# Optimization experiments

Measured on AMD Instinct MI355X. Metric: run time of the kernel, lower is better.

The kernel has to match this reference:

```python
import jax, jax.numpy as jnp
import numpy as np

NC = 1_000_000   # children
NP_ = 100_000    # parents
DIM = 64         # value/channel dim
H = 4            # heads
DQK = 8          # per-head query/key dim
DH = DQK * H     # 32
RPE = 9          # edge_attr feature dim
SCALE = DQK ** -0.5


def setup_inputs() -> dict:
    key = jax.random.key(0)
    ks = jax.random.split(key, 12)
    return {
        "x_child": jax.random.normal(ks[0], (NC, DIM), dtype=jnp.float32),
        "x_parent": jax.random.normal(ks[1], (NP_, DIM), dtype=jnp.float32),
        "index": jax.random.randint(ks[2], (NC,), 0, NP_, dtype=jnp.int64),
        "edge_attr": jax.random.normal(ks[3], (NC, RPE), dtype=jnp.float32),
        "wq": jax.random.normal(ks[4], (DIM, DH), dtype=jnp.float32) * 0.05,
        "bq": jax.random.normal(ks[5], (DH,), dtype=jnp.float32) * 0.05,
        "wkv": jax.random.normal(ks[6], (DIM, DH + DIM), dtype=jnp.float32) * 0.05,
        "bkv": jax.random.normal(ks[7], (DH + DIM,), dtype=jnp.float32) * 0.05,
        "wk_rpe": jax.random.normal(ks[8], (RPE, DH), dtype=jnp.float32) * 0.05,
        "bk_rpe": jax.random.normal(ks[9], (DH,), dtype=jnp.float32) * 0.05,
        "wq_rpe": jax.random.normal(ks[10], (RPE, DH), dtype=jnp.float32) * 0.05,
        "bq_rpe": jax.random.normal(ks[11], (DH,), dtype=jnp.float32) * 0.05,
    }


def reference(x_child, x_parent, index, edge_attr,
              wq, bq, wkv, bkv, wk_rpe, bk_rpe, wq_rpe, bq_rpe):
    Nc = x_child.shape[0]
    Np = x_parent.shape[0]
    # _get_query: Linear(Cp -> H*DQK) on parents, then gather per child edge
    q_parent = x_parent @ wq + bq                      # (Np, H*D)
    q = q_parent[index].reshape(Nc, H, DQK) * SCALE    # (Nc, H, D)
    # kv projection on children
    kv = x_child @ wkv + bkv                           # (Nc, H*D + DIM)
    k = kv[:, :DH].reshape(Nc, H, DQK)
    v = kv[:, DH:].reshape(Nc, H, DIM // H)
    # relative positional encodings added to k and q
    k = k + (edge_attr @ wk_rpe + bk_rpe).reshape(Nc, H, DQK)
    q = q + (edge_attr @ wq_rpe + bq_rpe).reshape(Nc, H, DQK)
    # per-edge compatibility, segment softmax grouped by parent index
    compat = jnp.einsum('nhd,nhd->nh', q, k)           # (Nc, H)
    m = jax.ops.segment_max(compat, index, num_segments=Np)   # (Np, H)
    e = jnp.exp(compat - m[index])
    s = jax.ops.segment_sum(e, index, num_segments=Np)        # (Np, H)
    attn = e / (s[index] + 1e-16)                      # (Nc, H)
    # weighted scatter-sum pooling
    xw = (v * attn[:, :, None]).reshape(Nc, DIM)       # (Nc, DIM)
    out = jax.ops.segment_sum(xw, index, num_segments=Np)     # (Np, DIM)
    return out
```

## Files before the change

kernel.cpp:

```cpp
#include <hip/hip_runtime.h>

#define NC    1000000
#define NPAR  100000
#define DIM   64
#define H     4
#define RPE   9
#define SCALE 0.35355339059327373f
#define CB    128
#define NBS   ((NPAR + 1023) / 1024)

typedef __attribute__((ext_vector_type(8))) short short8;
typedef __attribute__((ext_vector_type(4))) float f32x4;

__device__ inline unsigned short f2bf(float f) {
    unsigned int u = __float_as_uint(f);
    u += 0x7fff + ((u >> 16) & 1);
    return (unsigned short)(u >> 16);
}
__device__ inline unsigned int pack2bf(float a, float b) {
    return (unsigned int)f2bf(a) | ((unsigned int)f2bf(b) << 16);
}

__global__ __launch_bounds__(256) void qproj_kernel(const float* __restrict__ xp,
                             const float* __restrict__ wq,
                             const float* __restrict__ bq,
                             float* __restrict__ qp) {
    __shared__ float wqT[32 * 64];
    __shared__ float bqL[32];
    int tid = threadIdx.x;
    for (int i = tid; i < 2048; i += 256) { int o = i >> 6, j = i & 63; wqT[i] = wq[j * 32 + o]; }
    if (tid < 32) bqL[tid] = bq[tid];
    __syncthreads();
    int p = blockIdx.x * 256 + tid;
    if (p >= NPAR) return;
    float4 x4[16];
    const float4* xr = (const float4*)(xp + (size_t)p * 64);
#pragma unroll
    for (int i = 0; i < 16; ++i) x4[i] = xr[i];
    float* qpr = qp + (size_t)p * 32;
#pragma unroll 1
    for (int o = 0; o < 32; ++o) {
        float acc = bqL[o];
        const float4* w4 = (const float4*)(wqT + o * 64);
#pragma unroll
        for (int j = 0; j < 16; ++j) { float4 w = w4[j], xx = x4[j];
            acc += xx.x * w.x + xx.y * w.y + xx.z * w.z + xx.w * w.w; }
        qpr[o] = acc * SCALE;
    }
}

__global__ __launch_bounds__(256) void prepB_kernel(
    const float* __restrict__ wkv, const float* __restrict__ bkv,
    const float* __restrict__ wkr, const float* __restrict__ bkr,
    const float* __restrict__ wqr, const float* __restrict__ bqr,
    uint4* __restrict__ Bg) {
    int tid = threadIdx.x;
    for (int i = tid; i < 12 * 128; i += 256) {
        int kb = i >> 7, n = i & 127;
        float w[8];
#pragma unroll
        for (int jj = 0; jj < 8; ++jj) {
            int k = kb * 8 + jj;
            float val = 0.f;
            if (n < 32) {
                if (k < 64)       val = wkv[k * 96 + n];
                else if (k < 73)  val = wkr[(k - 64) * 32 + n];
                else if (k == 73) val = bkv[n] + bkr[n];
            } else if (n < 96) {
                int d = n - 32;
                if (k < 64)       val = wkv[k * 96 + 32 + d];
                else if (k == 73) val = bkv[32 + d];
            } else {
                int o = n - 96;
                if (k >= 64 && k < 73) val = wqr[(k - 64) * 32 + o];
                else if (k == 73)      val = bqr[o];
            }
            w[jj] = val;
        }
        uint4 v;
        v.x = pack2bf(w[0], w[1]); v.y = pack2bf(w[2], w[3]);
        v.z = pack2bf(w[4], w[5]); v.w = pack2bf(w[6], w[7]);
        Bg[kb * 128 + n] = v;
    }
}

__global__ __launch_bounds__(256) void hist_kernel(const int* __restrict__ index,
                            int* __restrict__ cnt) {
    int c = blockIdx.x * 256 + threadIdx.x;
    if (c >= NC) return;
    atomicAdd(&cnt[index[c]], 1);
}

__global__ __launch_bounds__(1024) void scanA_kernel(const int* __restrict__ cnt,
                                                     int* __restrict__ bsum) {
    __shared__ int red[16];
    int i = blockIdx.x * 1024 + threadIdx.x;
    int v = (i < NPAR) ? cnt[i] : 0;
#pragma unroll
    for (int off = 32; off; off >>= 1) v += __shfl_down(v, off, 64);
    if ((threadIdx.x & 63) == 0) red[threadIdx.x >> 6] = v;
    __syncthreads();
    if (threadIdx.x < 16) {
        int s = red[threadIdx.x];
#pragma unroll
        for (int off = 8; off; off >>= 1) s += __shfl_down(s, off, 16);
        if (threadIdx.x == 0) bsum[blockIdx.x] = s;
    }
}

__global__ __launch_bounds__(128) void scanB_kernel(int* __restrict__ bsum) {
    __shared__ int s[128];
    int t = threadIdx.x;
    int v = (t < NBS) ? bsum[t] : 0;
    s[t] = v;
    __syncthreads();
    for (int off = 1; off < 128; off <<= 1) {
        int x = s[t];
        int add = (t >= off) ? s[t - off] : 0;
        __syncthreads();
        s[t] = x + add;
        __syncthreads();
    }
    if (t < NBS) bsum[t] = s[t] - v;
}

__global__ __launch_bounds__(1024) void scanC_kernel(const int* __restrict__ cnt,
                                                     const int* __restrict__ bsum,
                                                     int* __restrict__ rowStart,
                                                     int* __restrict__ cursor) {
    __shared__ int s[1024];
    int t = threadIdx.x;
    int i = blockIdx.x * 1024 + t;
    int v = (i < NPAR) ? cnt[i] : 0;
    s[t] = v;
    __syncthreads();
    for (int off = 1; off < 1024; off <<= 1) {
        int x = s[t];
        int add = (t >= off) ? s[t - off] : 0;
        __syncthreads();
        s[t] = x + add;
        __syncthreads();
    }
    int excl = s[t] - v + bsum[blockIdx.x];
    if (i < NPAR) { rowStart[i] = excl; cursor[i] = excl; }
    if (i == NPAR - 1) rowStart[NPAR] = excl + v;
}

__global__ __launch_bounds__(256) void scatter_kernel(const int* __restrict__ index,
                               int* __restrict__ cursor,
                               int2* __restrict__ ordCP) {
    int c = blockIdx.x * 256 + threadIdx.x;
    if (c >= NC) return;
    int p = index[c];
    int pos = atomicAdd(&cursor[p], 1);
    ordCP[pos] = make_int2(c, p);
}

__global__ __launch_bounds__(256, 4) void fused_kernel(
    const float* __restrict__ xc, const float* __restrict__ ea_g,
    const int2* __restrict__ ordCP,
    const int* __restrict__ rowStart,
    const uint4* __restrict__ Bg,
    const float* __restrict__ qp,
    float* __restrict__ outw, float* __restrict__ sW)
{
    __shared__ __align__(16) char R1[34816];
    __shared__ float e_lds[CB * 4];
    __shared__ int par_s[CB];
    __shared__ int wcnt[4];
    __shared__ int segStart[130];

    uint4* A4 = (uint4*)R1;
    float* wvS = (float*)R1;

    const int tid  = threadIdx.x;
    const int lane = tid & 63, wave = tid >> 6;
    const int col  = lane & 15, quad = lane >> 4;
    const int G    = blockIdx.x * CB;
    const int validCB = min(NC - G, CB);

    {
        const int half = tid >> 7;
        const int c = tid & 127;
        const bool valid = c < validCB;
        int ch = 0, p = 0x7fffffff;
        if (valid) { int2 cp = ordCP[G + c]; ch = cp.x; p = cp.y; }
        if (half == 0) {
            par_s[c] = p;
            float4 x4[10];
            if (valid) {
                const float4* xr = (const float4*)(xc + (size_t)ch * 64);
#pragma unroll
                for (int i = 0; i < 10; ++i) x4[i] = xr[i];
            } else {
#pragma unroll
                for (int i = 0; i < 10; ++i) x4[i] = make_float4(0.f, 0.f, 0.f, 0.f);
            }
#pragma unroll
            for (int kb = 0; kb < 5; ++kb) {
                uint4 v;
                v.x = pack2bf(x4[kb * 2].x, x4[kb * 2].y);
                v.y = pack2bf(x4[kb * 2].z, x4[kb * 2].w);
                v.z = pack2bf(x4[kb * 2 + 1].x, x4[kb * 2 + 1].y);
                v.w = pack2bf(x4[kb * 2 + 1].z, x4[kb * 2 + 1].w);
                A4[kb * 128 + c] = v;
            }
        } else {
            float4 x4[6];
            float ear[9];
            if (valid) {
                const float4* xr = (const float4*)(xc + (size_t)ch * 64);
#pragma unroll
                for (int i = 0; i < 6; ++i) x4[i] = xr[10 + i];
                const float* er = ea_g + (size_t)ch * 9;
#pragma unroll
                for (int r = 0; r < 9; ++r) ear[r] = er[r];
            } else {
#pragma unroll
                for (int i = 0; i < 6; ++i) x4[i] = make_float4(0.f, 0.f, 0.f, 0.f);
#pragma unroll
                for (int r = 0; r < 9; ++r) ear[r] = 0.f;
            }
#pragma unroll
            for (int kb = 0; kb < 3; ++kb) {
                uint4 v;
                v.x = pack2bf(x4[kb * 2].x, x4[kb * 2].y);
                v.y = pack2bf(x4[kb * 2].z, x4[kb * 2].w);
                v.z = pack2bf(x4[kb * 2 + 1].x, x4[kb * 2 + 1].y);
                v.w = pack2bf(x4[kb * 2 + 1].z, x4[kb * 2 + 1].w);
                A4[(5 + kb) * 128 + c] = v;
            }
            {
                uint4 v;
                v.x = pack2bf(ear[0], ear[1]); v.y = pack2bf(ear[2], ear[3]);
                v.z = pack2bf(ear[4], ear[5]); v.w = pack2bf(ear[6], ear[7]);
                A4[8 * 128 + c] = v;
            }
            {
                uint4 v;
                v.x = pack2bf(ear[8], valid ? 1.f : 0.f);
                v.y = 0u; v.z = 0u; v.w = 0u;
                A4[9 * 128 + c] = v;
            }
        }
    }
    __syncthreads();

    f32x4 acc[2][8];
#pragma unroll
    for (int mt = 0; mt < 2; ++mt)
#pragma unroll
        for (int nt = 0; nt < 8; ++nt) acc[mt][nt] = (f32x4){0.f, 0.f, 0.f, 0.f};
    const int wbase = wave * 32;
    const short8* As = (const short8*)A4;
    const short8* Bs = (const short8*)Bg;
    const short8 zero8 = {0, 0, 0, 0, 0, 0, 0, 0};
#pragma unroll 1
    for (int ks = 0; ks < 3; ++ks) {
        const int kb = ks * 4 + quad;
        short8 af0 = zero8, af1 = zero8;
        if (kb < 10) {
            af0 = As[kb * 128 + wbase + col];
            af1 = As[kb * 128 + wbase + 16 + col];
        }
        short8 bf[8];
#pragma unroll
        for (int nt = 0; nt < 6; ++nt) bf[nt] = Bs[kb * 128 + nt * 16 + col];
#pragma unroll
        for (int nt = 0; nt < 6; ++nt) {
            acc[0][nt] = __builtin_amdgcn_mfma_f32_16x16x32_bf16(af0, bf[nt], acc[0][nt], 0, 0, 0);
            acc[1][nt] = __builtin_amdgcn_mfma_f32_16x16x32_bf16(af1, bf[nt], acc[1][nt], 0, 0, 0);
        }
        if (ks == 2) {
#pragma unroll
            for (int nt = 6; nt < 8; ++nt) {
                short8 b2 = Bs[kb * 128 + nt * 16 + col];
                acc[0][nt] = __builtin_amdgcn_mfma_f32_16x16x32_bf16(af0, b2, acc[0][nt], 0, 0, 0);
                acc[1][nt] = __builtin_amdgcn_mfma_f32_16x16x32_bf16(af1, b2, acc[1][nt], 0, 0, 0);
            }
        }
    }
    __syncthreads();

    {
        float comp[2][4][2];
#pragma unroll
        for (int mt = 0; mt < 2; ++mt) {
#pragma unroll
            for (int r = 0; r < 4; ++r) {
                int cc = wbase + mt * 16 + quad * 4 + r;
                int p = par_s[cc];
                if (p >= NPAR) p = 0;
                const float* qpr = qp + (size_t)p * 32;
#pragma unroll
                for (int nt = 0; nt < 2; ++nt) {
                    float q = qpr[nt * 16 + col] + acc[mt][nt + 6][r];
                    comp[mt][r][nt] = acc[mt][nt][r] * q;
                }
            }
        }
#pragma unroll
        for (int m = 1; m < 8; m <<= 1) {
#pragma unroll
            for (int mt = 0; mt < 2; ++mt)
#pragma unroll
                for (int r = 0; r < 4; ++r)
#pragma unroll
                    for (int nt = 0; nt < 2; ++nt)
                        comp[mt][r][nt] += __shfl_xor(comp[mt][r][nt], m, 64);
        }
        {
            int idx = col & 7;
            int mtS = idx >> 2, rS = idx & 3;
            int cS = wbase + mtS * 16 + quad * 4 + rS;
            int hb = col >> 3;
            bool v0 = cS < validCB;
            e_lds[cS * 4 + hb]     = v0 ? __expf(comp[mtS][rS][0]) : 0.f;
            e_lds[cS * 4 + 2 + hb] = v0 ? __expf(comp[mtS][rS][1]) : 0.f;
        }
        const int c = tid;
        bool valid = (c < validCB);
        bool ishead = valid && (c == 0 || par_s[c - 1] != par_s[c]);
        unsigned long long mask = __ballot(ishead);
        if (lane == 0) wcnt[wave] = __popcll(mask);
        __syncthreads();
        int base = 0;
#pragma unroll
        for (int w = 0; w < 4; ++w) if (w < wave) base += wcnt[w];
        if (ishead) segStart[base + __popcll(mask & ((1ull << lane) - 1))] = c;
        if (tid == 0) {
            int ns = wcnt[0] + wcnt[1] + wcnt[2] + wcnt[3];
            segStart[ns] = validCB;
            segStart[129] = ns;
        }
    }

#pragma unroll
    for (int mt = 0; mt < 2; ++mt) {
        int cb = wbase + mt * 16 + quad * 4;
#pragma unroll
        for (int nt = 2; nt < 6; ++nt) {
            int d = (nt - 2) * 16 + col;
            int h = nt - 2;
#pragma unroll
            for (int r = 0; r < 4; ++r) {
                float e = e_lds[(cb + r) * 4 + h];
                wvS[(cb + r) * 68 + d] = acc[mt][nt][r] * e;
            }
        }
    }
    __syncthreads();

    {
        int nseg = segStart[129];
        for (int s = wave; s < nseg; s += 4) {
            int a = segStart[s], b = segStart[s + 1];
            int p = par_s[a];
            int d = lane, h = lane >> 4;
            float vs = 0.f, es = 0.f;
            for (int c2 = a; c2 < b; ++c2) {
                vs += wvS[c2 * 68 + d];
                es += e_lds[c2 * 4 + h];
            }
            bool full = (rowStart[p] == G + a) && (rowStart[p + 1] == G + b);
            if (full) {
                outw[(size_t)p * 64 + d] = vs;
                if ((d & 15) == 0) sW[(size_t)p * 4 + h] = es;
            } else {
                atomicAdd(&outw[(size_t)p * 64 + d], vs);
                if ((d & 15) == 0) atomicAdd(&sW[(size_t)p * 4 + h], es);
            }
        }
    }
}

__global__ __launch_bounds__(256) void norm_kernel(const float* __restrict__ sW,
                                                   float* __restrict__ out) {
    int t = blockIdx.x * 256 + threadIdx.x;
    if (t >= NPAR * 64) return;
    out[t] = out[t] / (sW[(t >> 6) * 4 + ((t >> 4) & 3)] + 1e-16f);
}

extern "C" void kernel_launch(void* const* d_in, const int* in_sizes, int n_in,
                              void* d_out, int out_size, void* d_ws, size_t ws_size,
                              hipStream_t stream) {
    const float* xc   = (const float*)d_in[0];
    const float* xp   = (const float*)d_in[1];
    const int*   idx  = (const int*)d_in[2];
    const float* ea   = (const float*)d_in[3];
    const float* wq   = (const float*)d_in[4];
    const float* bq   = (const float*)d_in[5];
    const float* wkv  = (const float*)d_in[6];
    const float* bkv  = (const float*)d_in[7];
    const float* wkr  = (const float*)d_in[8];
    const float* bkr  = (const float*)d_in[9];
    const float* wqr  = (const float*)d_in[10];
    const float* bqr  = (const float*)d_in[11];
    float* out = (float*)d_out;

    char* base = (char*)d_ws;
    size_t off = 0;
    auto alloc = [&](size_t bytes) {
        void* r = base + off;
        off += (bytes + 255) & ~(size_t)255;
        return r;
    };
    float* qp       = (float*)alloc((size_t)NPAR * 32 * sizeof(float));
    int*   cnt      = (int*)  alloc((size_t)NPAR * sizeof(int));
    int*   rowStart = (int*)  alloc(((size_t)NPAR + 1) * sizeof(int));
    int*   cursor   = (int*)  alloc((size_t)NPAR * sizeof(int));
    int2*  ordCP    = (int2*) alloc((size_t)NC * sizeof(int2));
    float* sW       = (float*)alloc((size_t)NPAR * 4 * sizeof(float));
    int*   bsum     = (int*)  alloc((size_t)NBS * sizeof(int));
    uint4* Bg       = (uint4*)alloc((size_t)12 * 128 * sizeof(uint4));
    (void)ws_size;

    hipMemsetAsync(cnt, 0, (size_t)NPAR * sizeof(int), stream);
    hipMemsetAsync(sW,  0, (size_t)NPAR * 4 * sizeof(float), stream);
    hipMemsetAsync(out, 0, (size_t)NPAR * 64 * sizeof(float), stream);

    qproj_kernel  <<<(NPAR + 255) / 256, 256, 0, stream>>>(xp, wq, bq, qp);
    prepB_kernel  <<<1,                  256, 0, stream>>>(wkv, bkv, wkr, bkr, wqr, bqr, Bg);
    hist_kernel   <<<(NC + 255) / 256,   256, 0, stream>>>(idx, cnt);
    scanA_kernel  <<<NBS,               1024, 0, stream>>>(cnt, bsum);
    scanB_kernel  <<<1,                  128, 0, stream>>>(bsum);
    scanC_kernel  <<<NBS,               1024, 0, stream>>>(cnt, bsum, rowStart, cursor);
    scatter_kernel<<<(NC + 255) / 256,   256, 0, stream>>>(idx, cursor, ordCP);
    fused_kernel  <<<(NC + CB - 1) / CB, 256, 0, stream>>>(xc, ea, ordCP, rowStart,
                                                           Bg, qp, out, sW);
    norm_kernel   <<<(NPAR * 64 + 255) / 256, 256, 0, stream>>>(sW, out);
}
```

Before: 677.9 us.

## Make fused kernel persistent with register prefetch of next tile's gathered rows

The fused attention kernel now runs as a persistent grid of 1024 blocks that loop over 128-child tiles. While the MFMA and epilogue work for the current tile runs, the next tile's ordCP entry, child features and edge attributes are loaded and packed to bf16 in registers. This is meant to hide the latency of the random-row gather behind compute. In exchange it raises register pressure, which may lower occupancy, and adds a barrier at the end of each tile.

```diff
diff --git a/kernel.cpp b/kernel.cpp
--- a/kernel.cpp
+++ b/kernel.cpp
@@ -8,6 +8,8 @@
 #define SCALE 0.35355339059327373f
 #define CB    128
 #define NBS   ((NPAR + 1023) / 1024)
+#define NT_TILES ((NC + CB - 1) / CB)
+#define GRID_F 1024
 
 typedef __attribute__((ext_vector_type(8))) short short8;
 typedef __attribute__((ext_vector_type(4))) float f32x4;
@@ -176,201 +178,257 @@
     const int tid  = threadIdx.x;
     const int lane = tid & 63, wave = tid >> 6;
     const int col  = lane & 15, quad = lane >> 4;
-    const int G    = blockIdx.x * CB;
-    const int validCB = min(NC - G, CB);
+    const int c    = tid & 127;
+    const int half = tid >> 7;
+    const int wbase = wave * 32;
+    const short8 zero8 = {0, 0, 0, 0, 0, 0, 0, 0};
+
+    int t = blockIdx.x;
+    int2 cp;
+    uint4 pk[5];
 
     {
-        const int half = tid >> 7;
-        const int c = tid & 127;
-        const bool valid = c < validCB;
-        int ch = 0, p = 0x7fffffff;
-        if (valid) { int2 cp = ordCP[G + c]; ch = cp.x; p = cp.y; }
+        int g = t * CB + c;
+        bool v = g < NC;
+        int2 cl = ordCP[v ? g : 0];
+        if (!v) { cl.x = 0; cl.y = 0x7fffffff; }
+        int ch = cl.x;
+        float4 xa[10]; float ear[9];
         if (half == 0) {
-            par_s[c] = p;
-            float4 x4[10];
-            if (valid) {
-                const float4* xr = (const float4*)(xc + (size_t)ch * 64);
-#pragma unroll
-                for (int i = 0; i < 10; ++i) x4[i] = xr[i];
-            } else {
-#pragma unroll
-                for (int i = 0; i < 10; ++i) x4[i] = make_float4(0.f, 0.f, 0.f, 0.f);
-            }
+            const float4* xr = (const float4*)(xc + (size_t)ch * 64);
+#pragma unroll
+            for (int i = 0; i < 10; ++i) xa[i] = xr[i];
 #pragma unroll
             for (int kb = 0; kb < 5; ++kb) {
-                uint4 v;
-                v.x = pack2bf(x4[kb * 2].x, x4[kb * 2].y);
-                v.y = pack2bf(x4[kb * 2].z, x4[kb * 2].w);
-                v.z = pack2bf(x4[kb * 2 + 1].x, x4[kb * 2 + 1].y);
-                v.w = pack2bf(x4[kb * 2 + 1].z, x4[kb * 2 + 1].w);
-                A4[kb * 128 + c] = v;
+                uint4 u;
+                u.x = pack2bf(xa[kb*2].x,   xa[kb*2].y);
+                u.y = pack2bf(xa[kb*2].z,   xa[kb*2].w);
+                u.z = pack2bf(xa[kb*2+1].x, xa[kb*2+1].y);
+                u.w = pack2bf(xa[kb*2+1].z, xa[kb*2+1].w);
+                pk[kb] = v ? u : make_uint4(0u,0u,0u,0u);
             }
         } else {
-            float4 x4[6];
-            float ear[9];
-            if (valid) {
-                const float4* xr = (const float4*)(xc + (size_t)ch * 64);
-#pragma unroll
-                for (int i = 0; i < 6; ++i) x4[i] = xr[10 + i];
-                const float* er = ea_g + (size_t)ch * 9;
-#pragma unroll
-                for (int r = 0; r < 9; ++r) ear[r] = er[r];
-            } else {
-#pragma unroll
-                for (int i = 0; i < 6; ++i) x4[i] = make_float4(0.f, 0.f, 0.f, 0.f);
-#pragma unroll
-                for (int r = 0; r < 9; ++r) ear[r] = 0.f;
-            }
+            const float4* xr = (const float4*)(xc + (size_t)ch * 64);
+#pragma unroll
+            for (int i = 0; i < 6; ++i) xa[i] = xr[10 + i];
+            const float* er = ea_g + (size_t)ch * 9;
+#pragma unroll
+            for (int r = 0; r < 9; ++r) ear[r] = er[r];
 #pragma unroll
             for (int kb = 0; kb < 3; ++kb) {
-                uint4 v;
-                v.x = pack2bf(x4[kb * 2].x, x4[kb * 2].y);
-                v.y = pack2bf(x4[kb * 2].z, x4[kb * 2].w);
-                v.z = pack2bf(x4[kb * 2 + 1].x, x4[kb * 2 + 1].y);
-                v.w = pack2bf(x4[kb * 2 + 1].z, x4[kb * 2 + 1].w);
-                A4[(5 + kb) * 128 + c] = v;
-            }
-            {
-                uint4 v;
-                v.x = pack2bf(ear[0], ear[1]); v.y = pack2bf(ear[2], ear[3]);
-                v.z = pack2bf(ear[4], ear[5]); v.w = pack2bf(ear[6], ear[7]);
-                A4[8 * 128 + c] = v;
-            }
-            {
-                uint4 v;
-                v.x = pack2bf(ear[8], valid ? 1.f : 0.f);
-                v.y = 0u; v.z = 0u; v.w = 0u;
-                A4[9 * 128 + c] = v;
-            }
-        }
-    }
-    __syncthreads();
-
-    f32x4 acc[2][8];
-#pragma unroll
-    for (int mt = 0; mt < 2; ++mt)
-#pragma unroll
-        for (int nt = 0; nt < 8; ++nt) acc[mt][nt] = (f32x4){0.f, 0.f, 0.f, 0.f};
-    const int wbase = wave * 32;
-    const short8* As = (const short8*)A4;
-    const short8* Bs = (const short8*)Bg;
-    const short8 zero8 = {0, 0, 0, 0, 0, 0, 0, 0};
-#pragma unroll 1
-    for (int ks = 0; ks < 3; ++ks) {
-        const int kb = ks * 4 + quad;
-        short8 af0 = zero8, af1 = zero8;
-        if (kb < 10) {
-            af0 = As[kb * 128 + wbase + col];
-            af1 = As[kb * 128 + wbase + 16 + col];
-        }
-        short8 bf[8];
-#pragma unroll
-        for (int nt = 0; nt < 6; ++nt) bf[nt] = Bs[kb * 128 + nt * 16 + col];
-#pragma unroll
-        for (int nt = 0; nt < 6; ++nt) {
-            acc[0][nt] = __builtin_amdgcn_mfma_f32_16x16x32_bf16(af0, bf[nt], acc[0][nt], 0, 0, 0);
-            acc[1][nt] = __builtin_amdgcn_mfma_f32_16x16x32_bf16(af1, bf[nt], acc[1][nt], 0, 0, 0);
-        }
-        if (ks == 2) {
-#pragma unroll
-            for (int nt = 6; nt < 8; ++nt) {
-                short8 b2 = Bs[kb * 128 + nt * 16 + col];
-                acc[0][nt] = __builtin_amdgcn_mfma_f32_16x16x32_bf16(af0, b2, acc[0][nt], 0, 0, 0);
-                acc[1][nt] = __builtin_amdgcn_mfma_f32_16x16x32_bf16(af1, b2, acc[1][nt], 0, 0, 0);
-            }
-        }
-    }
-    __syncthreads();
-
-    {
-        float comp[2][4][2];
+                uint4 u;
+                u.x = pack2bf(xa[kb*2].x,   xa[kb*2].y);
+                u.y = pack2bf(xa[kb*2].z,   xa[kb*2].w);
+                u.z = pack2bf(xa[kb*2+1].x, xa[kb*2+1].y);
+                u.w = pack2bf(xa[kb*2+1].z, xa[kb*2+1].w);
+                pk[kb] = v ? u : make_uint4(0u,0u,0u,0u);
+            }
+            uint4 u8;
+            u8.x = pack2bf(ear[0], ear[1]); u8.y = pack2bf(ear[2], ear[3]);
+            u8.z = pack2bf(ear[4], ear[5]); u8.w = pack2bf(ear[6], ear[7]);
+            pk[3] = v ? u8 : make_uint4(0u,0u,0u,0u);
+            uint4 u9;
+            u9.x = pack2bf(ear[8], 1.f); u9.y = 0u; u9.z = 0u; u9.w = 0u;
+            pk[4] = v ? u9 : make_uint4(0u,0u,0u,0u);
+        }
+        cp = cl;
+    }
+
+    for (; t < NT_TILES; t += GRID_F) {
+        const int G = t * CB;
+        const int validCB = min(NC - G, CB);
+
+        int tn = (t + GRID_F < NT_TILES) ? (t + GRID_F) : t;
+        int gn = tn * CB + c;
+        bool vn = gn < NC;
+        int2 cpn = ordCP[vn ? gn : 0];
+
+        if (half == 0) {
+            par_s[c] = cp.y;
+#pragma unroll
+            for (int kb = 0; kb < 5; ++kb) A4[kb * 128 + c] = pk[kb];
+        } else {
+#pragma unroll
+            for (int kb = 0; kb < 5; ++kb) A4[(5 + kb) * 128 + c] = pk[kb];
+        }
+        __syncthreads();
+
+        f32x4 acc[2][8];
+#pragma unroll
+        for (int mt = 0; mt < 2; ++mt)
+#pragma unroll
+            for (int nt = 0; nt < 8; ++nt) acc[mt][nt] = (f32x4){0.f, 0.f, 0.f, 0.f};
+        const short8* As = (const short8*)A4;
+        const short8* Bs = (const short8*)Bg;
+#pragma unroll
+        for (int ks = 0; ks < 3; ++ks) {
+            const int kb = ks * 4 + quad;
+            short8 af0 = zero8, af1 = zero8;
+            if (kb < 10) {
+                af0 = As[kb * 128 + wbase + col];
+                af1 = As[kb * 128 + wbase + 16 + col];
+            }
+            short8 bf[4];
+#pragma unroll
+            for (int nt = 0; nt < 4; ++nt) bf[nt] = Bs[kb * 128 + nt * 16 + col];
+#pragma unroll
+            for (int nt = 0; nt < 4; ++nt) {
+                acc[0][nt] = __builtin_amdgcn_mfma_f32_16x16x32_bf16(af0, bf[nt], acc[0][nt], 0, 0, 0);
+                acc[1][nt] = __builtin_amdgcn_mfma_f32_16x16x32_bf16(af1, bf[nt], acc[1][nt], 0, 0, 0);
+            }
+            bf[0] = Bs[kb * 128 + 4 * 16 + col];
+            bf[1] = Bs[kb * 128 + 5 * 16 + col];
+            acc[0][4] = __builtin_amdgcn_mfma_f32_16x16x32_bf16(af0, bf[0], acc[0][4], 0, 0, 0);
+            acc[1][4] = __builtin_amdgcn_mfma_f32_16x16x32_bf16(af1, bf[0], acc[1][4], 0, 0, 0);
+            acc[0][5] = __builtin_amdgcn_mfma_f32_16x16x32_bf16(af0, bf[1], acc[0][5], 0, 0, 0);
+            acc[1][5] = __builtin_amdgcn_mfma_f32_16x16x32_bf16(af1, bf[1], acc[1][5], 0, 0, 0);
+            if (ks == 2) {
+                bf[2] = Bs[kb * 128 + 6 * 16 + col];
+                bf[3] = Bs[kb * 128 + 7 * 16 + col];
+                acc[0][6] = __builtin_amdgcn_mfma_f32_16x16x32_bf16(af0, bf[2], acc[0][6], 0, 0, 0);
+                acc[1][6] = __builtin_amdgcn_mfma_f32_16x16x32_bf16(af1, bf[2], acc[1][6], 0, 0, 0);
+                acc[0][7] = __builtin_amdgcn_mfma_f32_16x16x32_bf16(af0, bf[3], acc[0][7], 0, 0, 0);
+                acc[1][7] = __builtin_amdgcn_mfma_f32_16x16x32_bf16(af1, bf[3], acc[1][7], 0, 0, 0);
+            }
+        }
+
+        int chn = vn ? cpn.x : 0;
+        float4 xa[10]; float ear[9];
+        if (half == 0) {
+            const float4* xr = (const float4*)(xc + (size_t)chn * 64);
+#pragma unroll
+            for (int i = 0; i < 10; ++i) xa[i] = xr[i];
+        } else {
+            const float4* xr = (const float4*)(xc + (size_t)chn * 64);
+#pragma unroll
+            for (int i = 0; i < 6; ++i) xa[i] = xr[10 + i];
+            const float* er = ea_g + (size_t)chn * 9;
+#pragma unroll
+            for (int r = 0; r < 9; ++r) ear[r] = er[r];
+        }
+
 #pragma unroll
         for (int mt = 0; mt < 2; ++mt) {
+            float comp[4][2];
 #pragma unroll
             for (int r = 0; r < 4; ++r) {
                 int cc = wbase + mt * 16 + quad * 4 + r;
                 int p = par_s[cc];
-                if (p >= NPAR) p = 0;
+                p = (p < NPAR) ? p : 0;
                 const float* qpr = qp + (size_t)p * 32;
 #pragma unroll
-                for (int nt = 0; nt < 2; ++nt) {
-                    float q = qpr[nt * 16 + col] + acc[mt][nt + 6][r];
-                    comp[mt][r][nt] = acc[mt][nt][r] * q;
+                for (int nt = 0; nt < 2; ++nt)
+                    comp[r][nt] = acc[mt][nt][r] * (qpr[nt * 16 + col] + acc[mt][nt + 6][r]);
+            }
+#pragma unroll
+            for (int m = 1; m < 8; m <<= 1)
+#pragma unroll
+                for (int r = 0; r < 4; ++r)
+#pragma unroll
+                    for (int nt = 0; nt < 2; ++nt)
+                        comp[r][nt] += __shfl_xor(comp[r][nt], m, 64);
+            int collo = lane & 7, colhi = (lane >> 3) & 1;
+            float eArg = comp[0][0];
+            eArg = (collo == 1) ? comp[1][0] : eArg;
+            eArg = (collo == 2) ? comp[2][0] : eArg;
+            eArg = (collo == 3) ? comp[3][0] : eArg;
+            eArg = (collo == 4) ? comp[0][1] : eArg;
+            eArg = (collo == 5) ? comp[1][1] : eArg;
+            eArg = (collo == 6) ? comp[2][1] : eArg;
+            eArg = (collo == 7) ? comp[3][1] : eArg;
+            int rS = collo & 3, ntS = collo >> 2;
+            int cS = wbase + mt * 16 + quad * 4 + rS;
+            float eV = (cS < validCB) ? __expf(eArg) : 0.f;
+            e_lds[cS * 4 + ntS * 2 + colhi] = eV;
+        }
+
+        if (half == 0) {
+#pragma unroll
+            for (int kb = 0; kb < 5; ++kb) {
+                uint4 u;
+                u.x = pack2bf(xa[kb*2].x,   xa[kb*2].y);
+                u.y = pack2bf(xa[kb*2].z,   xa[kb*2].w);
+                u.z = pack2bf(xa[kb*2+1].x, xa[kb*2+1].y);
+                u.w = pack2bf(xa[kb*2+1].z, xa[kb*2+1].w);
+                pk[kb] = vn ? u : make_uint4(0u,0u,0u,0u);
+            }
+        } else {
+#pragma unroll
+            for (int kb = 0; kb < 3; ++kb) {
+                uint4 u;
+                u.x = pack2bf(xa[kb*2].x,   xa[kb*2].y);
+                u.y = pack2bf(xa[kb*2].z,   xa[kb*2].w);
+                u.z = pack2bf(xa[kb*2+1].x, xa[kb*2+1].y);
+                u.w = pack2bf(xa[kb*2+1].z, xa[kb*2+1].w);
+                pk[kb] = vn ? u : make_uint4(0u,0u,0u,0u);
+            }
+            uint4 u8;
+            u8.x = pack2bf(ear[0], ear[1]); u8.y = pack2bf(ear[2], ear[3]);
+            u8.z = pack2bf(ear[4], ear[5]); u8.w = pack2bf(ear[6], ear[7]);
+            pk[3] = vn ? u8 : make_uint4(0u,0u,0u,0u);
+            uint4 u9;
+            u9.x = pack2bf(ear[8], 1.f); u9.y = 0u; u9.z = 0u; u9.w = 0u;
+            pk[4] = vn ? u9 : make_uint4(0u,0u,0u,0u);
+        }
+        cp.x = chn; cp.y = vn ? cpn.y : 0x7fffffff;
+
+        {
+            bool valid = (c == tid) && (tid < validCB);
+            bool vld = (tid < validCB);
+            bool ishead = vld && (tid == 0 || par_s[tid - 1] != par_s[tid]);
+            (void)valid;
+            unsigned long long mask = __ballot(ishead);
+            if (lane == 0) wcnt[wave] = __popcll(mask);
+            __syncthreads();
+            int base = 0;
+#pragma unroll
+            for (int w = 0; w < 4; ++w) if (w < wave) base += wcnt[w];
+            if (ishead) segStart[base + __popcll(mask & ((1ull << lane) - 1))] = tid;
+            if (tid == 0) {
+                int ns = wcnt[0] + wcnt[1] + wcnt[2] + wcnt[3];
+                segStart[ns] = validCB;
+                segStart[129] = ns;
+            }
+        }
+
+#pragma unroll
+        for (int mt = 0; mt < 2; ++mt) {
+            int cb = wbase + mt * 16 + quad * 4;
+#pragma unroll
+            for (int nt = 2; nt < 6; ++nt) {
+                int d = (nt - 2) * 16 + col;
+                int h = nt - 2;
+#pragma unroll
+                for (int r = 0; r < 4; ++r) {
+                    float e = e_lds[(cb + r) * 4 + h];
+                    wvS[(cb + r) * 68 + d] = acc[mt][nt][r] * e;
                 }
             }
         }
-#pragma unroll
-        for (int m = 1; m < 8; m <<= 1) {
-#pragma unroll
-            for (int mt = 0; mt < 2; ++mt)
-#pragma unroll
-                for (int r = 0; r < 4; ++r)
-#pragma unroll
-                    for (int nt = 0; nt < 2; ++nt)
-                        comp[mt][r][nt] += __shfl_xor(comp[mt][r][nt], m, 64);
-        }
+        __syncthreads();
+
         {
-            int idx = col & 7;
-            int mtS = idx >> 2, rS = idx & 3;
-            int cS = wbase + mtS * 16 + quad * 4 + rS;
-            int hb = col >> 3;
-            bool v0 = cS < validCB;
-            e_lds[cS * 4 + hb]     = v0 ? __expf(comp[mtS][rS][0]) : 0.f;
-            e_lds[cS * 4 + 2 + hb] = v0 ? __expf(comp[mtS][rS][1]) : 0.f;
-        }
-        const int c = tid;
-        bool valid = (c < validCB);
-        bool ishead = valid && (c == 0 || par_s[c - 1] != par_s[c]);
-        unsigned long long mask = __ballot(ishead);
-        if (lane == 0) wcnt[wave] = __popcll(mask);
-        __syncthreads();
-        int base = 0;
-#pragma unroll
-        for (int w = 0; w < 4; ++w) if (w < wave) base += wcnt[w];
-        if (ishead) segStart[base + __popcll(mask & ((1ull << lane) - 1))] = c;
-        if (tid == 0) {
-            int ns = wcnt[0] + wcnt[1] + wcnt[2] + wcnt[3];
-            segStart[ns] = validCB;
-            segStart[129] = ns;
-        }
-    }
-
-#pragma unroll
-    for (int mt = 0; mt < 2; ++mt) {
-        int cb = wbase + mt * 16 + quad * 4;
-#pragma unroll
-        for (int nt = 2; nt < 6; ++nt) {
-            int d = (nt - 2) * 16 + col;
-            int h = nt - 2;
-#pragma unroll
-            for (int r = 0; r < 4; ++r) {
-                float e = e_lds[(cb + r) * 4 + h];
-                wvS[(cb + r) * 68 + d] = acc[mt][nt][r] * e;
-            }
-        }
-    }
-    __syncthreads();
-
-    {
-        int nseg = segStart[129];
-        for (int s = wave; s < nseg; s += 4) {
-            int a = segStart[s], b = segStart[s + 1];
-            int p = par_s[a];
-            int d = lane, h = lane >> 4;
-            float vs = 0.f, es = 0.f;
-            for (int c2 = a; c2 < b; ++c2) {
-                vs += wvS[c2 * 68 + d];
-                es += e_lds[c2 * 4 + h];
-            }
-            bool full = (rowStart[p] == G + a) && (rowStart[p + 1] == G + b);
-            if (full) {
-                outw[(size_t)p * 64 + d] = vs;
-                if ((d & 15) == 0) sW[(size_t)p * 4 + h] = es;
-            } else {
-                atomicAdd(&outw[(size_t)p * 64 + d], vs);
-                if ((d & 15) == 0) atomicAdd(&sW[(size_t)p * 4 + h], es);
-            }
-        }
+            int nseg = segStart[129];
+            for (int s = wave; s < nseg; s += 4) {
+                int a = segStart[s], b = segStart[s + 1];
+                int p = par_s[a];
+                int d = lane, h = lane >> 4;
+                float vs = 0.f, es = 0.f;
+                for (int c2 = a; c2 < b; ++c2) {
+                    vs += wvS[c2 * 68 + d];
+                    es += e_lds[c2 * 4 + h];
+                }
+                bool full = (rowStart[p] == G + a) && (rowStart[p + 1] == G + b);
+                if (full) {
+                    outw[(size_t)p * 64 + d] = vs;
+                    if ((d & 15) == 0) sW[(size_t)p * 4 + h] = es;
+                } else {
+                    atomicAdd(&outw[(size_t)p * 64 + d], vs);
+                    if ((d & 15) == 0) atomicAdd(&sW[(size_t)p * 4 + h], es);
+                }
+            }
+        }
+        __syncthreads();
     }
 }
 
@@ -426,7 +484,7 @@
     scanB_kernel  <<<1,                  128, 0, stream>>>(bsum);
     scanC_kernel  <<<NBS,               1024, 0, stream>>>(cnt, bsum, rowStart, cursor);
     scatter_kernel<<<(NC + 255) / 256,   256, 0, stream>>>(idx, cursor, ordCP);
-    fused_kernel  <<<(NC + CB - 1) / CB, 256, 0, stream>>>(xc, ea, ordCP, rowStart,
+    fused_kernel  <<<GRID_F,             256, 0, stream>>>(xc, ea, ordCP, rowStart,
                                                            Bg, qp, out, sW);
     norm_kernel   <<<(NPAR * 64 + 255) / 256, 256, 0, stream>>>(sW, out);
 }
```

New measurement: 0.9996 ms. +47.5%, slower.
